# Kernel optimization log

Hardware: AMD Instinct MI355X
Metric: run time of the kernel (lower is better)

The kernel has to match this reference:

```python
import jax, jax.numpy as jnp
import numpy as np

NUM_GRAPHS = 1024
NODES_PER_GRAPH = 116
DEG = 32
IN_CH = 116
HID = 32
EPS = 1e-5


def setup_inputs() -> dict:
    key = jax.random.key(0)
    ks = jax.random.split(key, 16)
    N = NUM_GRAPHS * NODES_PER_GRAPH
    E = N * DEG
    x = jax.random.normal(ks[0], (N, IN_CH), dtype=jnp.float32)
    # edges stay within each graph: graph id per edge, then random src/dst node in that graph
    gid = jnp.arange(E, dtype=jnp.int64) // (NODES_PER_GRAPH * DEG)
    off = gid * NODES_PER_GRAPH
    src = off + jax.random.randint(ks[1], (E,), 0, NODES_PER_GRAPH, dtype=jnp.int64)
    dst = off + jax.random.randint(ks[2], (E,), 0, NODES_PER_GRAPH, dtype=jnp.int64)
    edge_index = jnp.stack([src, dst], axis=0)
    edge_weight = jax.random.uniform(ks[3], (E,), dtype=jnp.float32)
    batch = jnp.arange(N, dtype=jnp.int64) // NODES_PER_GRAPH
    xavier = lambda k, fi, fo: jax.random.uniform(k, (fi, fo), jnp.float32, -1.0, 1.0) * np.sqrt(6.0 / (fi + fo))
    return {
        "x": x, "edge_index": edge_index, "edge_weight": edge_weight, "batch": batch,
        "W1": xavier(ks[4], IN_CH, HID), "b1": jnp.zeros((HID,), jnp.float32),
        "g1": jnp.ones((HID,), jnp.float32), "be1": jnp.zeros((HID,), jnp.float32),
        "W2": xavier(ks[5], HID, 2 * HID), "b2": jnp.zeros((2 * HID,), jnp.float32),
        "g2": jnp.ones((2 * HID,), jnp.float32), "be2": jnp.zeros((2 * HID,), jnp.float32),
        "Wf1": xavier(ks[6], 4 * HID, HID), "bf1": jnp.zeros((HID,), jnp.float32),
        "gf": jnp.ones((HID,), jnp.float32), "bef": jnp.zeros((HID,), jnp.float32),
        "Wf2": xavier(ks[7], HID, 2), "bf2": jnp.zeros((2,), jnp.float32),
    }


def _gcn_conv(x, row, col, ew, W, b):
    """PyG GCNConv: linear -> add self-loops -> sym-normalized scatter-add -> +bias."""
    N = x.shape[0]
    h = x @ W  # [N, out]
    loop = jnp.arange(N, dtype=row.dtype)
    row_sl = jnp.concatenate([row, loop])
    col_sl = jnp.concatenate([col, loop])
    w_sl = jnp.concatenate([ew, jnp.ones((N,), ew.dtype)])
    deg = jax.ops.segment_sum(w_sl, col_sl, num_segments=N)
    dinv = jnp.where(deg > 0, jax.lax.rsqrt(deg), 0.0)
    norm = dinv[row_sl] * w_sl * dinv[col_sl]  # [E+N]
    msg = h[row_sl] * norm[:, None]            # gather + scale
    out = jax.ops.segment_sum(msg, col_sl, num_segments=N)
    return out + b


def _bn(x, g, b):
    # BatchNorm1d in training mode: biased batch stats over axis 0
    m = jnp.mean(x, axis=0)
    v = jnp.mean(jnp.square(x - m), axis=0)
    return (x - m) * jax.lax.rsqrt(v + EPS) * g + b


def reference(x, edge_index, edge_weight, batch, W1, b1, g1, be1, W2, b2, g2, be2,
              Wf1, bf1, gf, bef, Wf2, bf2):
    row, col = edge_index[0], edge_index[1]
    h = jax.nn.relu(_bn(_gcn_conv(x, row, col, edge_weight, W1, b1), g1, be1))
    h = jax.nn.relu(_bn(_gcn_conv(h, row, col, edge_weight, W2, b2), g2, be2))
    # global mean / max pool over graphs
    counts = jax.ops.segment_sum(jnp.ones((h.shape[0],), h.dtype), batch, num_segments=NUM_GRAPHS)
    x_mean = jax.ops.segment_sum(h, batch, num_segments=NUM_GRAPHS) / counts[:, None]
    x_max = jax.ops.segment_max(h, batch, num_segments=NUM_GRAPHS)
    emb = jnp.concatenate([x_mean, x_max], axis=1)  # [G, 4*HID]
    z = jax.nn.relu(_bn(emb @ Wf1 + bf1, gf, bef))  # dropout = identity (eval)
    return z @ Wf2 + bf2  # [G, num_classes]
```

## Files before the change

### kernel.cpp

```cpp
#include <hip/hip_runtime.h>

#define NPG 116
#define EPG (NPG * 32)
#define HID 32
#define HID2 64
#define EPS 1e-5f

#define AS 136
#define YSS 40
#define HPG 7424

using bf16x8 = __attribute__((ext_vector_type(8))) short;
using f32x4  = __attribute__((ext_vector_type(4))) float;

__device__ __forceinline__ unsigned short f2bf(float f) {
  union { float f; unsigned int i; } cv;
  cv.f = f;
  unsigned int x = cv.i;
  x += 0x7fff + ((x >> 16) & 1);
  return (unsigned short)(x >> 16);
}

#define MFMA16(a, b, c) __builtin_amdgcn_mfma_f32_16x16x32_bf16((a), (b), (c), 0, 0, 0)


__global__ __launch_bounds__(1024) void k_build(const int* __restrict__ ei,
                                                const float* __restrict__ ew,
                                                float* __restrict__ dinvg,
                                                float* __restrict__ buf,
                                                int N, int E) {
  __shared__ float Wf[NPG * NPG];
  __shared__ float degs[NPG];
  const int g = blockIdx.x, tid = threadIdx.x;
  const int nb = g * NPG, e0 = g * EPG;
  const int* rowp = ei;
  const int* colp = ei + E;

  for (int i = tid; i < NPG; i += 1024) degs[i] = 1.0f;
  { float4* p = (float4*)Wf;
    for (int i = tid; i < NPG * 29; i += 1024) p[i] = make_float4(0,0,0,0); }
  __syncthreads();

  for (int e = tid; e < EPG; e += 1024) {
    int eg = e0 + e;
    int s = rowp[eg] - nb, d = colp[eg] - nb;
    float wv = ew[eg];
    atomicAdd(&degs[d], wv);
    atomicAdd(&Wf[d * NPG + s], wv);
  }
  if (tid < NPG) atomicAdd(&Wf[tid * NPG + tid], 1.0f);
  __syncthreads();

  if (tid < NPG) dinvg[nb + tid] = rsqrtf(degs[tid]);
  int* wbg = (int*)(buf + (size_t)g * HPG);
  for (int idx = tid; idx < NPG * 64; idx += 1024) {
    int r = idx >> 6, jj = idx & 63;
    int val = 0;
    if (jj < 58) {
      float2 v = *(const float2*)&Wf[r * NPG + 2 * jj];
      val = (unsigned)f2bf(v.x) | ((unsigned)f2bf(v.y) << 16);
    }
    wbg[idx] = val;
  }
}

__global__ __launch_bounds__(256) void k_conv1(const float* __restrict__ x,
                                               const float* __restrict__ W1,
                                               const float* __restrict__ dinvg,
                                               const float* __restrict__ buf,
                                               float* __restrict__ h1,
                                               float* __restrict__ stats,
                                               int N) {
  __shared__ __align__(16) short W1T[HID * AS];
  __shared__ __align__(16) short L1T[HID * AS];
  __shared__ float dv[NPG];
  __shared__ float ss[HID], qs[HID];
  const int g = blockIdx.x, tid = threadIdx.x;
  const int nb = g * NPG;
  const int l = tid & 63, w = tid >> 6;
  const int rf = l & 15, kg = l >> 4;

  if (tid < HID) { ss[tid] = 0.0f; qs[tid] = 0.0f; }
  for (int i = tid; i < NPG; i += 256) dv[i] = dinvg[nb + i];
  for (int i = tid; i < HID * 20; i += 256) {
    int c = i / 20, k = 116 + (i - 20 * (i / 20));
    W1T[c * AS + k] = 0;
    L1T[c * AS + k] = 0;
  }
  for (int i = tid; i < NPG * HID; i += 256) {
    int k = i >> 5, c = i & 31;
    W1T[c * AS + k] = (short)f2bf(W1[i]);
  }
  __syncthreads();

#pragma unroll
  for (int mi = 0; mi < 2; ++mi) {
    const int mt = w + 4 * mi;
    const int rl = mt * 16 + rf;
    f32x4 a0 = {0.f,0.f,0.f,0.f}, a1 = {0.f,0.f,0.f,0.f};
#pragma unroll
    for (int kk = 0; kk < 4; ++kk) {
      bf16x8 a;
      if (rl < NPG) {
        const float* xr = x + (size_t)(nb + rl) * NPG;
        if (kk < 3) {
          const float4* xp = (const float4*)(xr + kk * 32 + kg * 8);
          float4 v0 = xp[0], v1 = xp[1];
          a[0] = (short)f2bf(v0.x); a[1] = (short)f2bf(v0.y);
          a[2] = (short)f2bf(v0.z); a[3] = (short)f2bf(v0.w);
          a[4] = (short)f2bf(v1.x); a[5] = (short)f2bf(v1.y);
          a[6] = (short)f2bf(v1.z); a[7] = (short)f2bf(v1.w);
        } else {
          const int k0 = 96 + kg * 8;
#pragma unroll
          for (int j = 0; j < 8; ++j) {
            int k = k0 + j;
            a[j] = (k < NPG) ? (short)f2bf(xr[k]) : (short)0;
          }
        }
      } else {
#pragma unroll
        for (int j = 0; j < 8; ++j) a[j] = 0;
      }
      bf16x8 b0 = *(const bf16x8*)&W1T[rf * AS + kk * 32 + kg * 8];
      bf16x8 b1 = *(const bf16x8*)&W1T[(16 + rf) * AS + kk * 32 + kg * 8];
      a0 = MFMA16(a, b0, a0);
      a1 = MFMA16(a, b1, a1);
    }
#pragma unroll
    for (int i = 0; i < 4; ++i) {
      int row = mt * 16 + kg * 4 + i;
      if (row < NPG) {
        float dr = dv[row];
        L1T[rf * AS + row] = (short)f2bf(dr * a0[i]);
        L1T[(16 + rf) * AS + row] = (short)f2bf(dr * a1[i]);
      }
    }
  }
  __syncthreads();

  const unsigned short* wbs =
      (const unsigned short*)(buf + (size_t)g * HPG);
  float s0 = 0.f, q0 = 0.f, s1 = 0.f, q1 = 0.f;
#pragma unroll
  for (int mi = 0; mi < 2; ++mi) {
    const int mt = w + 4 * mi;
    const int rl = mt * 16 + rf;
    f32x4 a0 = {0.f,0.f,0.f,0.f}, a1 = {0.f,0.f,0.f,0.f};
#pragma unroll
    for (int kk = 0; kk < 4; ++kk) {
      bf16x8 a;
      if (rl < NPG) {
        a = *(const bf16x8*)&wbs[rl * 128 + kk * 32 + kg * 8];
      } else {
#pragma unroll
        for (int j = 0; j < 8; ++j) a[j] = 0;
      }
      bf16x8 b0 = *(const bf16x8*)&L1T[rf * AS + kk * 32 + kg * 8];
      bf16x8 b1 = *(const bf16x8*)&L1T[(16 + rf) * AS + kk * 32 + kg * 8];
      a0 = MFMA16(a, b0, a0);
      a1 = MFMA16(a, b1, a1);
    }
#pragma unroll
    for (int i = 0; i < 4; ++i) {
      int row = mt * 16 + kg * 4 + i;
      if (row < NPG) {
        float dr = dv[row];
        float v0 = dr * a0[i], v1 = dr * a1[i];
        float* hrow = h1 + (size_t)(nb + row) * HID;
        hrow[rf] = v0;
        hrow[16 + rf] = v1;
        s0 += v0; q0 += v0 * v0;
        s1 += v1; q1 += v1 * v1;
      }
    }
  }
  atomicAdd(&ss[rf], s0);      atomicAdd(&qs[rf], q0);
  atomicAdd(&ss[16 + rf], s1); atomicAdd(&qs[16 + rf], q1);
  __syncthreads();
  if (tid < HID) {
    atomicAdd(&stats[tid], ss[tid]);
    atomicAdd(&stats[32 + tid], qs[tid]);
  }
}

__global__ __launch_bounds__(512) void k_conv2(const float* __restrict__ h1,
                                               const float* __restrict__ W2,
                                               const float* __restrict__ g1,
                                               const float* __restrict__ be1,
                                               const float* __restrict__ stats,
                                               const float* __restrict__ dinvg,
                                               float* __restrict__ buf,
                                               float* __restrict__ stats2,
                                               float invN, int N) {
  __shared__ __align__(16) short ysb[128 * YSS];
  __shared__ __align__(16) short W2T[HID2 * YSS];
  __shared__ __align__(16) short L2T[HID2 * AS];
  __shared__ float dv[NPG];
  __shared__ float ss[HID2], qs[HID2];
  __shared__ float a1s[HID], c1s[HID];
  const int g = blockIdx.x, tid = threadIdx.x;
  const int nb = g * NPG;
  const int l = tid & 63, w = tid >> 6;
  const int rf = l & 15, kg = l >> 4;
  float* bufg = buf + (size_t)g * HPG;

  if (tid < HID) {
    float m = stats[tid] * invN;
    float v = stats[32 + tid] * invN - m * m;
    float a = g1[tid] * rsqrtf(v + EPS);
    a1s[tid] = a;
    c1s[tid] = be1[tid] - m * a;
  }
  if (tid < HID2) { ss[tid] = 0.0f; qs[tid] = 0.0f; }
  { int* p = (int*)ysb;
    for (int i = tid; i < 128 * YSS / 2; i += 512) p[i] = 0; }
  { int* p = (int*)L2T;
    for (int i = tid; i < HID2 * AS / 2; i += 512) p[i] = 0; }
  for (int i = tid; i < HID * HID2; i += 512) {
    int k = i >> 6, c = i & 63;
    W2T[c * YSS + k] = (short)f2bf(W2[i]);
  }
  for (int i = tid; i < NPG; i += 512) dv[i] = dinvg[nb + i];
  __syncthreads();

  {
    const float4* hg = (const float4*)(h1 + (size_t)nb * HID);
    for (int i = tid; i < NPG * 8; i += 512) {
      int r = i >> 3, kc = i & 7, k0 = kc * 4;
      float4 hv = hg[i];
      float dr = dv[r];
      float y0 = dr * fmaxf(0.f, a1s[k0 + 0] * hv.x + c1s[k0 + 0]);
      float y1 = dr * fmaxf(0.f, a1s[k0 + 1] * hv.y + c1s[k0 + 1]);
      float y2 = dr * fmaxf(0.f, a1s[k0 + 2] * hv.z + c1s[k0 + 2]);
      float y3 = dr * fmaxf(0.f, a1s[k0 + 3] * hv.w + c1s[k0 + 3]);
      unsigned int* yp = (unsigned int*)&ysb[r * YSS + k0];
      yp[0] = (unsigned)f2bf(y0) | ((unsigned)f2bf(y1) << 16);
      yp[1] = (unsigned)f2bf(y2) | ((unsigned)f2bf(y3) << 16);
    }
  }
  __syncthreads();

#pragma unroll
  for (int u = 0; u < 4; ++u) {
    const int t = w + 8 * u;
    const int mt = t >> 2, nt = t & 3;
    bf16x8 a = *(const bf16x8*)&ysb[(mt * 16 + rf) * YSS + kg * 8];
    bf16x8 b = *(const bf16x8*)&W2T[(nt * 16 + rf) * YSS + kg * 8];
    f32x4 acc = {0.f, 0.f, 0.f, 0.f};
    acc = MFMA16(a, b, acc);
    const int col = nt * 16 + rf;
#pragma unroll
    for (int i = 0; i < 4; ++i) {
      int row = mt * 16 + kg * 4 + i;
      if (row < NPG) L2T[col * AS + row] = (short)f2bf(acc[i]);
    }
  }
  __syncthreads();

  {
    const unsigned short* wbs = (const unsigned short*)bufg;
    const int mt = w;
    const int rl = mt * 16 + rf;
    f32x4 acc[4];
#pragma unroll
    for (int nt = 0; nt < 4; ++nt) acc[nt] = (f32x4){0.f, 0.f, 0.f, 0.f};
#pragma unroll
    for (int kk = 0; kk < 4; ++kk) {
      bf16x8 a;
      if (rl < NPG) {
        a = *(const bf16x8*)&wbs[rl * 128 + kk * 32 + kg * 8];
      } else {
#pragma unroll
        for (int j = 0; j < 8; ++j) a[j] = 0;
      }
#pragma unroll
      for (int nt = 0; nt < 4; ++nt) {
        bf16x8 b = *(const bf16x8*)&L2T[(nt * 16 + rf) * AS + kk * 32 + kg * 8];
        acc[nt] = MFMA16(a, b, acc[nt]);
      }
    }
#pragma unroll
    for (int nt = 0; nt < 4; ++nt) {
      const int col = nt * 16 + rf;
      float s_ = 0.f, q_ = 0.f;
#pragma unroll
      for (int i = 0; i < 4; ++i) {
        int row = mt * 16 + kg * 4 + i;
        if (row < NPG) {
          float v = dv[row] * acc[nt][i];
          bufg[row * HID2 + col] = v;
          s_ += v; q_ += v * v;
        }
      }
      atomicAdd(&ss[col], s_);
      atomicAdd(&qs[col], q_);
    }
  }
  __syncthreads();
  if (tid < HID2) {
    atomicAdd(&stats2[tid], ss[tid]);
    atomicAdd(&stats2[64 + tid], qs[tid]);
  }
}

__global__ __launch_bounds__(256) void k_pool(const float* __restrict__ buf,
                                              const float* __restrict__ g2,
                                              const float* __restrict__ be2,
                                              const float* __restrict__ stats2,
                                              const float* __restrict__ Wf1,
                                              float* __restrict__ z,
                                              float invN, int N) {
  __shared__ float4 psum4[256], pmax4[256];
  __shared__ __align__(16) float emb[128];
  __shared__ __align__(16) float a2s[HID2], c2s[HID2];
  int g = blockIdx.x, tid = threadIdx.x;
  if (tid < HID2) {
    float m = stats2[tid] * invN;
    float v = stats2[64 + tid] * invN - m * m;
    float a = g2[tid] * rsqrtf(v + EPS);
    a2s[tid] = a;
    c2s[tid] = be2[tid] - m * a;
  }
  __syncthreads();
  int c4 = tid & 15, rg = tid >> 4;
  float4 av = ((const float4*)a2s)[c4], bv = ((const float4*)c2s)[c4];
  const float4* h4 = (const float4*)(buf + (size_t)g * HPG);
  float4 s = {0.f, 0.f, 0.f, 0.f};
  float4 mx = {-1e30f, -1e30f, -1e30f, -1e30f};
  for (int n = rg; n < NPG; n += 16) {
    float4 v = h4[n * 16 + c4];
    float4 y;
    y.x = fmaxf(0.f, av.x * v.x + bv.x);
    y.y = fmaxf(0.f, av.y * v.y + bv.y);
    y.z = fmaxf(0.f, av.z * v.z + bv.z);
    y.w = fmaxf(0.f, av.w * v.w + bv.w);
    s.x += y.x; s.y += y.y; s.z += y.z; s.w += y.w;
    mx.x = fmaxf(mx.x, y.x); mx.y = fmaxf(mx.y, y.y);
    mx.z = fmaxf(mx.z, y.z); mx.w = fmaxf(mx.w, y.w);
  }
  psum4[rg * 16 + c4] = s;
  pmax4[rg * 16 + c4] = mx;
  __syncthreads();
  if (tid < 16) {
    float4 S = psum4[tid], M = pmax4[tid];
    for (int j = 1; j < 16; ++j) {
      float4 p = psum4[j * 16 + tid], q = pmax4[j * 16 + tid];
      S.x += p.x; S.y += p.y; S.z += p.z; S.w += p.w;
      M.x = fmaxf(M.x, q.x); M.y = fmaxf(M.y, q.y);
      M.z = fmaxf(M.z, q.z); M.w = fmaxf(M.w, q.w);
    }
    const float inv = 1.0f / NPG;
    ((float4*)emb)[tid] = make_float4(S.x * inv, S.y * inv, S.z * inv, S.w * inv);
    ((float4*)emb)[16 + tid] = M;
  }
  __syncthreads();
  if (tid < 32) {
    float acc = 0.0f;
#pragma unroll
    for (int k = 0; k < 128; ++k) acc += emb[k] * Wf1[k * 32 + tid];
    z[g * 32 + tid] = acc;
  }
}

__global__ __launch_bounds__(256) void k_final(const float* __restrict__ z,
                                               const float* __restrict__ gf,
                                               const float* __restrict__ bef,
                                               const float* __restrict__ Wf2,
                                               const float* __restrict__ bf2,
                                               float* __restrict__ out, int G) {
  __shared__ float ss[32], qs[32], af[32], cf[32];
  __shared__ float w2s[64], b2s[2];
  int tid = threadIdx.x;
  if (tid < 32) { ss[tid] = 0.0f; qs[tid] = 0.0f; }
  if (tid < 64) w2s[tid] = Wf2[tid];
  if (tid < 2) b2s[tid] = bf2[tid];
  __syncthreads();
  const float4* z4 = (const float4*)z;
  int n4 = G * 8;
  float4 s = {0.f, 0.f, 0.f, 0.f}, q = {0.f, 0.f, 0.f, 0.f};
  for (int i = tid; i < n4; i += 256) {
    float4 v = z4[i];
    s.x += v.x; s.y += v.y; s.z += v.z; s.w += v.w;
    q.x += v.x * v.x; q.y += v.y * v.y; q.z += v.z * v.z; q.w += v.w * v.w;
  }
  int cg = (tid & 7) * 4;
  atomicAdd(&ss[cg + 0], s.x); atomicAdd(&ss[cg + 1], s.y);
  atomicAdd(&ss[cg + 2], s.z); atomicAdd(&ss[cg + 3], s.w);
  atomicAdd(&qs[cg + 0], q.x); atomicAdd(&qs[cg + 1], q.y);
  atomicAdd(&qs[cg + 2], q.z); atomicAdd(&qs[cg + 3], q.w);
  __syncthreads();
  if (tid < 32) {
    float invG = 1.0f / G;
    float m = ss[tid] * invG;
    float v = qs[tid] * invG - m * m;
    float a = gf[tid] * rsqrtf(v + EPS);
    af[tid] = a;
    cf[tid] = bef[tid] - m * a;
  }
  __syncthreads();
  for (int g = tid; g < G; g += 256) {
    float o0 = b2s[0], o1 = b2s[1];
    const float4* zr = z4 + g * 8;
#pragma unroll
    for (int kc = 0; kc < 8; ++kc) {
      float4 v = zr[kc];
      int j = 4 * kc;
      float y;
      y = fmaxf(0.f, af[j + 0] * v.x + cf[j + 0]);
      o0 += y * w2s[2 * (j + 0)]; o1 += y * w2s[2 * (j + 0) + 1];
      y = fmaxf(0.f, af[j + 1] * v.y + cf[j + 1]);
      o0 += y * w2s[2 * (j + 1)]; o1 += y * w2s[2 * (j + 1) + 1];
      y = fmaxf(0.f, af[j + 2] * v.z + cf[j + 2]);
      o0 += y * w2s[2 * (j + 2)]; o1 += y * w2s[2 * (j + 2) + 1];
      y = fmaxf(0.f, af[j + 3] * v.w + cf[j + 3]);
      o0 += y * w2s[2 * (j + 3)]; o1 += y * w2s[2 * (j + 3) + 1];
    }
    out[g * 2] = o0;
    out[g * 2 + 1] = o1;
  }
}

extern "C" void kernel_launch(void* const* d_in, const int* in_sizes, int n_in,
                              void* d_out, int out_size, void* d_ws, size_t ws_size,
                              hipStream_t stream) {
  const float* x   = (const float*)d_in[0];
  const int*   ei  = (const int*)d_in[1];
  const float* ew  = (const float*)d_in[2];
  const float* W1  = (const float*)d_in[4];
  const float* g1  = (const float*)d_in[6];
  const float* be1 = (const float*)d_in[7];
  const float* W2  = (const float*)d_in[8];
  const float* g2  = (const float*)d_in[10];
  const float* be2 = (const float*)d_in[11];
  const float* Wf1 = (const float*)d_in[12];
  const float* gf  = (const float*)d_in[14];
  const float* bef = (const float*)d_in[15];
  const float* Wf2 = (const float*)d_in[16];
  const float* bf2 = (const float*)d_in[17];

  int N = in_sizes[3];
  int E = in_sizes[2];
  int G = N / NPG;

  float* ws    = (float*)d_ws;
  float* stats = ws;
  float* dinv  = ws + 256;
  float* h1    = dinv + N;
  float* buf   = h1 + (size_t)N * HID;
  float* z     = buf + (size_t)G * HPG;
  float* out   = (float*)d_out;
  float invN   = 1.0f / (float)N;

  hipMemsetAsync(stats, 0, 256 * sizeof(float), stream);
  k_build<<<G, 1024, 0, stream>>>(ei, ew, dinv, buf, N, E);
  k_conv1<<<G, 256, 0, stream>>>(x, W1, dinv, buf, h1, stats, N);
  k_conv2<<<G, 512, 0, stream>>>(h1, W2, g1, be1, stats, dinv, buf,
                                 stats + 64, invN, N);
  k_pool<<<G, 256, 0, stream>>>(buf, g2, be2, stats + 64, Wf1, z, invN, N);
  k_final<<<1, 256, 0, stream>>>(z, gf, bef, Wf2, bf2, out, G);
}
```

Baseline: 173.7 us.

## Prefetch global loads before LDS setup and widen conv1 to one tile per wave

In k_build, edge indices and weights are loaded into registers before shared memory is zeroed, and the bf16 adjacency is written with 16-byte stores instead of 4-byte stores. k_conv1 now launches 512 threads so each wave owns one 16-row tile, and it issues its x-row loads and adjacency-fragment loads before the shared-memory setup and barrier. k_conv2 likewise prefetches its adjacency A fragments into registers at kernel start. The aim is to hide global-memory latency behind LDS initialisation and to add parallelism, at the cost of more registers per thread.

```diff
diff --git a/kernel.cpp b/kernel.cpp
--- a/kernel.cpp
+++ b/kernel.cpp
@@ -36,35 +36,51 @@
   const int* rowp = ei;
   const int* colp = ei + E;
 
+  int sarr[4], darr[4];
+  float warr[4];
+#pragma unroll
+  for (int u = 0; u < 4; ++u) {
+    int e = tid + u * 1024;
+    bool ok = e < EPG;
+    sarr[u] = ok ? rowp[e0 + e] - nb : 0;
+    darr[u] = ok ? colp[e0 + e] - nb : 0;
+    warr[u] = ok ? ew[e0 + e] : 0.0f;
+  }
   for (int i = tid; i < NPG; i += 1024) degs[i] = 1.0f;
   { float4* p = (float4*)Wf;
     for (int i = tid; i < NPG * 29; i += 1024) p[i] = make_float4(0,0,0,0); }
   __syncthreads();
 
-  for (int e = tid; e < EPG; e += 1024) {
-    int eg = e0 + e;
-    int s = rowp[eg] - nb, d = colp[eg] - nb;
-    float wv = ew[eg];
-    atomicAdd(&degs[d], wv);
-    atomicAdd(&Wf[d * NPG + s], wv);
+#pragma unroll
+  for (int u = 0; u < 4; ++u) {
+    if (tid + u * 1024 < EPG) {
+      atomicAdd(&degs[darr[u]], warr[u]);
+      atomicAdd(&Wf[darr[u] * NPG + sarr[u]], warr[u]);
+    }
   }
   if (tid < NPG) atomicAdd(&Wf[tid * NPG + tid], 1.0f);
   __syncthreads();
 
   if (tid < NPG) dinvg[nb + tid] = rsqrtf(degs[tid]);
-  int* wbg = (int*)(buf + (size_t)g * HPG);
-  for (int idx = tid; idx < NPG * 64; idx += 1024) {
-    int r = idx >> 6, jj = idx & 63;
-    int val = 0;
-    if (jj < 58) {
-      float2 v = *(const float2*)&Wf[r * NPG + 2 * jj];
-      val = (unsigned)f2bf(v.x) | ((unsigned)f2bf(v.y) << 16);
-    }
-    wbg[idx] = val;
-  }
-}
-
-__global__ __launch_bounds__(256) void k_conv1(const float* __restrict__ x,
+  int4* wb4 = (int4*)(buf + (size_t)g * HPG);
+  for (int idx = tid; idx < NPG * 16; idx += 1024) {
+    int r = idx >> 4, j8 = (idx & 15) * 8;
+    float vb[8];
+#pragma unroll
+    for (int t = 0; t < 8; ++t) {
+      int c = j8 + t;
+      vb[t] = (c < NPG) ? Wf[r * NPG + c] : 0.0f;
+    }
+    int4 val;
+    val.x = (unsigned)f2bf(vb[0]) | ((unsigned)f2bf(vb[1]) << 16);
+    val.y = (unsigned)f2bf(vb[2]) | ((unsigned)f2bf(vb[3]) << 16);
+    val.z = (unsigned)f2bf(vb[4]) | ((unsigned)f2bf(vb[5]) << 16);
+    val.w = (unsigned)f2bf(vb[6]) | ((unsigned)f2bf(vb[7]) << 16);
+    wb4[idx] = val;
+  }
+}
+
+__global__ __launch_bounds__(512) void k_conv1(const float* __restrict__ x,
                                                const float* __restrict__ W1,
                                                const float* __restrict__ dinvg,
                                                const float* __restrict__ buf,
@@ -79,44 +95,52 @@
   const int nb = g * NPG;
   const int l = tid & 63, w = tid >> 6;
   const int rf = l & 15, kg = l >> 4;
-
+  const int mt = w, rl = mt * 16 + rf;
+
+  float4 xv[6];
+  float xt[8];
+  {
+    const float* xr = x + (size_t)(nb + (rl < NPG ? rl : 0)) * NPG;
+    const float4* xp4 = (const float4*)xr;
+#pragma unroll
+    for (int kk = 0; kk < 3; ++kk) {
+      xv[2 * kk]     = xp4[kk * 8 + kg * 2];
+      xv[2 * kk + 1] = xp4[kk * 8 + kg * 2 + 1];
+    }
+#pragma unroll
+    for (int j = 0; j < 8; ++j) {
+      int k = 96 + kg * 8 + j;
+      xt[j] = (k < NPG) ? xr[k] : 0.0f;
+    }
+  }
   if (tid < HID) { ss[tid] = 0.0f; qs[tid] = 0.0f; }
-  for (int i = tid; i < NPG; i += 256) dv[i] = dinvg[nb + i];
-  for (int i = tid; i < HID * 20; i += 256) {
+  for (int i = tid; i < NPG; i += 512) dv[i] = dinvg[nb + i];
+  for (int i = tid; i < HID * 20; i += 512) {
     int c = i / 20, k = 116 + (i - 20 * (i / 20));
     W1T[c * AS + k] = 0;
     L1T[c * AS + k] = 0;
   }
-  for (int i = tid; i < NPG * HID; i += 256) {
+  for (int i = tid; i < NPG * HID; i += 512) {
     int k = i >> 5, c = i & 31;
     W1T[c * AS + k] = (short)f2bf(W1[i]);
   }
   __syncthreads();
 
-#pragma unroll
-  for (int mi = 0; mi < 2; ++mi) {
-    const int mt = w + 4 * mi;
-    const int rl = mt * 16 + rf;
+  {
     f32x4 a0 = {0.f,0.f,0.f,0.f}, a1 = {0.f,0.f,0.f,0.f};
 #pragma unroll
     for (int kk = 0; kk < 4; ++kk) {
       bf16x8 a;
       if (rl < NPG) {
-        const float* xr = x + (size_t)(nb + rl) * NPG;
         if (kk < 3) {
-          const float4* xp = (const float4*)(xr + kk * 32 + kg * 8);
-          float4 v0 = xp[0], v1 = xp[1];
+          float4 v0 = xv[2 * kk], v1 = xv[2 * kk + 1];
           a[0] = (short)f2bf(v0.x); a[1] = (short)f2bf(v0.y);
           a[2] = (short)f2bf(v0.z); a[3] = (short)f2bf(v0.w);
           a[4] = (short)f2bf(v1.x); a[5] = (short)f2bf(v1.y);
           a[6] = (short)f2bf(v1.z); a[7] = (short)f2bf(v1.w);
         } else {
-          const int k0 = 96 + kg * 8;
-#pragma unroll
-          for (int j = 0; j < 8; ++j) {
-            int k = k0 + j;
-            a[j] = (k < NPG) ? (short)f2bf(xr[k]) : (short)0;
-          }
+#pragma unroll
+          for (int j = 0; j < 8; ++j) a[j] = (short)f2bf(xt[j]);
         }
       } else {
 #pragma unroll
@@ -137,30 +161,33 @@
       }
     }
   }
-  __syncthreads();
-
-  const unsigned short* wbs =
-      (const unsigned short*)(buf + (size_t)g * HPG);
-  float s0 = 0.f, q0 = 0.f, s1 = 0.f, q1 = 0.f;
-#pragma unroll
-  for (int mi = 0; mi < 2; ++mi) {
-    const int mt = w + 4 * mi;
-    const int rl = mt * 16 + rf;
+  bf16x8 av[4];
+  {
+    const unsigned short* wbs =
+        (const unsigned short*)(buf + (size_t)g * HPG);
+    const int rs = (rl < NPG ? rl : 0) * 128;
+#pragma unroll
+    for (int kk = 0; kk < 4; ++kk)
+      av[kk] = *(const bf16x8*)&wbs[rs + kk * 32 + kg * 8];
+    if (rl >= NPG) {
+#pragma unroll
+      for (int kk = 0; kk < 4; ++kk)
+#pragma unroll
+        for (int j = 0; j < 8; ++j) av[kk][j] = 0;
+    }
+  }
+  __syncthreads();
+
+  {
     f32x4 a0 = {0.f,0.f,0.f,0.f}, a1 = {0.f,0.f,0.f,0.f};
 #pragma unroll
     for (int kk = 0; kk < 4; ++kk) {
-      bf16x8 a;
-      if (rl < NPG) {
-        a = *(const bf16x8*)&wbs[rl * 128 + kk * 32 + kg * 8];
-      } else {
-#pragma unroll
-        for (int j = 0; j < 8; ++j) a[j] = 0;
-      }
       bf16x8 b0 = *(const bf16x8*)&L1T[rf * AS + kk * 32 + kg * 8];
       bf16x8 b1 = *(const bf16x8*)&L1T[(16 + rf) * AS + kk * 32 + kg * 8];
-      a0 = MFMA16(a, b0, a0);
-      a1 = MFMA16(a, b1, a1);
-    }
+      a0 = MFMA16(av[kk], b0, a0);
+      a1 = MFMA16(av[kk], b1, a1);
+    }
+    float s0 = 0.f, q0 = 0.f, s1 = 0.f, q1 = 0.f;
 #pragma unroll
     for (int i = 0; i < 4; ++i) {
       int row = mt * 16 + kg * 4 + i;
@@ -174,9 +201,9 @@
         s1 += v1; q1 += v1 * v1;
       }
     }
-  }
-  atomicAdd(&ss[rf], s0);      atomicAdd(&qs[rf], q0);
-  atomicAdd(&ss[16 + rf], s1); atomicAdd(&qs[16 + rf], q1);
+    atomicAdd(&ss[rf], s0);      atomicAdd(&qs[rf], q0);
+    atomicAdd(&ss[16 + rf], s1); atomicAdd(&qs[16 + rf], q1);
+  }
   __syncthreads();
   if (tid < HID) {
     atomicAdd(&stats[tid], ss[tid]);
@@ -204,7 +231,22 @@
   const int l = tid & 63, w = tid >> 6;
   const int rf = l & 15, kg = l >> 4;
   float* bufg = buf + (size_t)g * HPG;
-
+  const int mt = w, rl = mt * 16 + rf;
+
+  bf16x8 av[4];
+  {
+    const unsigned short* wbs = (const unsigned short*)bufg;
+    const int rs = (rl < NPG ? rl : 0) * 128;
+#pragma unroll
+    for (int kk = 0; kk < 4; ++kk)
+      av[kk] = *(const bf16x8*)&wbs[rs + kk * 32 + kg * 8];
+    if (rl >= NPG) {
+#pragma unroll
+      for (int kk = 0; kk < 4; ++kk)
+#pragma unroll
+        for (int j = 0; j < 8; ++j) av[kk][j] = 0;
+    }
+  }
   if (tid < HID) {
     float m = stats[tid] * invN;
     float v = stats[32 + tid] * invN - m * m;
@@ -244,40 +286,30 @@
 #pragma unroll
   for (int u = 0; u < 4; ++u) {
     const int t = w + 8 * u;
-    const int mt = t >> 2, nt = t & 3;
-    bf16x8 a = *(const bf16x8*)&ysb[(mt * 16 + rf) * YSS + kg * 8];
+    const int mt2 = t >> 2, nt = t & 3;
+    bf16x8 a = *(const bf16x8*)&ysb[(mt2 * 16 + rf) * YSS + kg * 8];
     bf16x8 b = *(const bf16x8*)&W2T[(nt * 16 + rf) * YSS + kg * 8];
     f32x4 acc = {0.f, 0.f, 0.f, 0.f};
     acc = MFMA16(a, b, acc);
     const int col = nt * 16 + rf;
 #pragma unroll
     for (int i = 0; i < 4; ++i) {
-      int row = mt * 16 + kg * 4 + i;
+      int row = mt2 * 16 + kg * 4 + i;
       if (row < NPG) L2T[col * AS + row] = (short)f2bf(acc[i]);
     }
   }
   __syncthreads();
 
   {
-    const unsigned short* wbs = (const unsigned short*)bufg;
-    const int mt = w;
-    const int rl = mt * 16 + rf;
     f32x4 acc[4];
 #pragma unroll
     for (int nt = 0; nt < 4; ++nt) acc[nt] = (f32x4){0.f, 0.f, 0.f, 0.f};
 #pragma unroll
     for (int kk = 0; kk < 4; ++kk) {
-      bf16x8 a;
-      if (rl < NPG) {
-        a = *(const bf16x8*)&wbs[rl * 128 + kk * 32 + kg * 8];
-      } else {
-#pragma unroll
-        for (int j = 0; j < 8; ++j) a[j] = 0;
-      }
 #pragma unroll
       for (int nt = 0; nt < 4; ++nt) {
         bf16x8 b = *(const bf16x8*)&L2T[(nt * 16 + rf) * AS + kk * 32 + kg * 8];
-        acc[nt] = MFMA16(a, b, acc[nt]);
+        acc[nt] = MFMA16(av[kk], b, acc[nt]);
       }
     }
 #pragma unroll
@@ -454,7 +486,7 @@
 
   hipMemsetAsync(stats, 0, 256 * sizeof(float), stream);
   k_build<<<G, 1024, 0, stream>>>(ei, ew, dinv, buf, N, E);
-  k_conv1<<<G, 256, 0, stream>>>(x, W1, dinv, buf, h1, stats, N);
+  k_conv1<<<G, 512, 0, stream>>>(x, W1, dinv, buf, h1, stats, N);
   k_conv2<<<G, 512, 0, stream>>>(h1, W2, g1, be1, stats, dinv, buf,
                                  stats + 64, invN, N);
   k_pool<<<G, 256, 0, stream>>>(buf, g2, be2, stats + 64, Wf1, z, invN, N);
```

After: 162.6 us. -6.4%, faster.

## Fuse all GNN stages into one cooperative kernel with register-resident activations

Applied to the files above, without the earlier changes.

Replaces the five-kernel pipeline with one cooperative kernel. Each 512-thread block handles four graphs and keeps the bf16 adjacency fragments and conv outputs in registers across stages, so the h1, h2, adjacency and z buffers no longer round-trip through global memory. Grid-wide syncs stand in for the kernel boundaries around the three batch-norm statistic reductions. In exchange it carries heavy register pressure, only 256 blocks in flight, and the cost of three grid barriers.

```diff
diff --git a/kernel.cpp b/kernel.cpp
--- a/kernel.cpp
+++ b/kernel.cpp
@@ -1,14 +1,15 @@
 #include <hip/hip_runtime.h>
+#include <hip/hip_cooperative_groups.h>
+namespace cg = cooperative_groups;
 
 #define NPG 116
 #define EPG (NPG * 32)
 #define HID 32
 #define HID2 64
 #define EPS 1e-5f
-
 #define AS 136
 #define YSS 40
-#define HPG 7424
+#define NG 4
 
 using bf16x8 = __attribute__((ext_vector_type(8))) short;
 using f32x4  = __attribute__((ext_vector_type(4))) float;
@@ -23,401 +24,333 @@
 
 #define MFMA16(a, b, c) __builtin_amdgcn_mfma_f32_16x16x32_bf16((a), (b), (c), 0, 0, 0)
 
-
-__global__ __launch_bounds__(1024) void k_build(const int* __restrict__ ei,
-                                                const float* __restrict__ ew,
-                                                float* __restrict__ dinvg,
-                                                float* __restrict__ buf,
-                                                int N, int E) {
-  __shared__ float Wf[NPG * NPG];
-  __shared__ float degs[NPG];
-  const int g = blockIdx.x, tid = threadIdx.x;
-  const int nb = g * NPG, e0 = g * EPG;
-  const int* rowp = ei;
-  const int* colp = ei + E;
-
-  for (int i = tid; i < NPG; i += 1024) degs[i] = 1.0f;
-  { float4* p = (float4*)Wf;
-    for (int i = tid; i < NPG * 29; i += 1024) p[i] = make_float4(0,0,0,0); }
-  __syncthreads();
-
-  for (int e = tid; e < EPG; e += 1024) {
-    int eg = e0 + e;
-    int s = rowp[eg] - nb, d = colp[eg] - nb;
-    float wv = ew[eg];
-    atomicAdd(&degs[d], wv);
-    atomicAdd(&Wf[d * NPG + s], wv);
-  }
-  if (tid < NPG) atomicAdd(&Wf[tid * NPG + tid], 1.0f);
-  __syncthreads();
-
-  if (tid < NPG) dinvg[nb + tid] = rsqrtf(degs[tid]);
-  int* wbg = (int*)(buf + (size_t)g * HPG);
-  for (int idx = tid; idx < NPG * 64; idx += 1024) {
-    int r = idx >> 6, jj = idx & 63;
-    int val = 0;
-    if (jj < 58) {
-      float2 v = *(const float2*)&Wf[r * NPG + 2 * jj];
-      val = (unsigned)f2bf(v.x) | ((unsigned)f2bf(v.y) << 16);
-    }
-    wbg[idx] = val;
-  }
-}
-
-__global__ __launch_bounds__(256) void k_conv1(const float* __restrict__ x,
-                                               const float* __restrict__ W1,
-                                               const float* __restrict__ dinvg,
-                                               const float* __restrict__ buf,
-                                               float* __restrict__ h1,
-                                               float* __restrict__ stats,
-                                               int N) {
+__global__ __launch_bounds__(512, 2) void k_fused(
+    const float* __restrict__ x, const int* __restrict__ ei,
+    const float* __restrict__ ew, const float* __restrict__ W1,
+    const float* __restrict__ W2, const float* __restrict__ Wf1,
+    const float* __restrict__ Wf2, const float* __restrict__ g1,
+    const float* __restrict__ be1, const float* __restrict__ g2,
+    const float* __restrict__ be2, const float* __restrict__ gf,
+    const float* __restrict__ bef, const float* __restrict__ bf2,
+    float* __restrict__ stats, float* __restrict__ out, int N, int E) {
+  __shared__ __align__(16) char regA[NPG * NPG * 4];
   __shared__ __align__(16) short W1T[HID * AS];
   __shared__ __align__(16) short L1T[HID * AS];
-  __shared__ float dv[NPG];
-  __shared__ float ss[HID], qs[HID];
-  const int g = blockIdx.x, tid = threadIdx.x;
-  const int nb = g * NPG;
+  __shared__ float dv[NG][NPG];
+  __shared__ float ssq[128];
+  __shared__ float cfs[256];
+  __shared__ float emb[NG][128];
+  __shared__ float zloc[NG * 32];
+  __shared__ float psum[64];
+  __shared__ int   pmaxi[64];
+
+  float* Wf  = (float*)regA;
+  short* ysb = (short*)regA;
+  short* W2T = (short*)(regA + 10240);
+  short* L2T = (short*)(regA + 15360);
+
+  cg::grid_group grid = cg::this_grid();
+  const int tid = threadIdx.x;
   const int l = tid & 63, w = tid >> 6;
   const int rf = l & 15, kg = l >> 4;
-
-  if (tid < HID) { ss[tid] = 0.0f; qs[tid] = 0.0f; }
-  for (int i = tid; i < NPG; i += 256) dv[i] = dinvg[nb + i];
-  for (int i = tid; i < HID * 20; i += 256) {
-    int c = i / 20, k = 116 + (i - 20 * (i / 20));
-    W1T[c * AS + k] = 0;
-    L1T[c * AS + k] = 0;
-  }
-  for (int i = tid; i < NPG * HID; i += 256) {
-    int k = i >> 5, c = i & 31;
-    W1T[c * AS + k] = (short)f2bf(W1[i]);
-  }
-  __syncthreads();
-
-#pragma unroll
-  for (int mi = 0; mi < 2; ++mi) {
-    const int mt = w + 4 * mi;
-    const int rl = mt * 16 + rf;
-    f32x4 a0 = {0.f,0.f,0.f,0.f}, a1 = {0.f,0.f,0.f,0.f};
+  const int rl = w * 16 + rf;
+  const bool rok = rl < NPG;
+  const int g0 = NG * blockIdx.x;
+  const float invN = 1.0f / (float)N;
+
+  for (int i = tid; i < HID * AS / 2; i += 512) {
+    ((int*)W1T)[i] = 0;
+    ((int*)L1T)[i] = 0;
+  }
+  __syncthreads();
+  for (int i = tid; i < NPG * 8; i += 512) {
+    int k = i >> 3, c4 = (i & 7) * 4;
+    float4 v = ((const float4*)W1)[i];
+    W1T[(c4 + 0) * AS + k] = (short)f2bf(v.x);
+    W1T[(c4 + 1) * AS + k] = (short)f2bf(v.y);
+    W1T[(c4 + 2) * AS + k] = (short)f2bf(v.z);
+    W1T[(c4 + 3) * AS + k] = (short)f2bf(v.w);
+  }
+
+  bf16x8 av[NG][4];
+  f32x4 h1a[NG][2];
+
+#pragma unroll
+  for (int gi = 0; gi < NG; ++gi) {
+    const int g = g0 + gi, nb = g * NPG, e0 = g * EPG;
+    float* degs = emb[gi];
+    for (int i = tid; i < NPG; i += 512) degs[i] = 1.0f;
+    { float4* p = (float4*)Wf;
+      for (int i = tid; i < NPG * 29; i += 512) p[i] = make_float4(0,0,0,0); }
+    __syncthreads();
+    for (int vi = tid; vi < EPG / 4; vi += 512) {
+      int4 s4 = ((const int4*)(ei + e0))[vi];
+      int4 d4 = ((const int4*)(ei + E + e0))[vi];
+      float4 w4 = ((const float4*)(ew + e0))[vi];
+      atomicAdd(&degs[d4.x - nb], w4.x);
+      atomicAdd(&Wf[(d4.x - nb) * NPG + (s4.x - nb)], w4.x);
+      atomicAdd(&degs[d4.y - nb], w4.y);
+      atomicAdd(&Wf[(d4.y - nb) * NPG + (s4.y - nb)], w4.y);
+      atomicAdd(&degs[d4.z - nb], w4.z);
+      atomicAdd(&Wf[(d4.z - nb) * NPG + (s4.z - nb)], w4.z);
+      atomicAdd(&degs[d4.w - nb], w4.w);
+      atomicAdd(&Wf[(d4.w - nb) * NPG + (s4.w - nb)], w4.w);
+    }
+    if (tid < NPG) atomicAdd(&Wf[tid * (NPG + 1)], 1.0f);
+    __syncthreads();
+    if (tid < NPG) dv[gi][tid] = rsqrtf(degs[tid]);
+
 #pragma unroll
     for (int kk = 0; kk < 4; ++kk) {
+      int off = kk * 32 + kg * 8;
       bf16x8 a;
-      if (rl < NPG) {
-        const float* xr = x + (size_t)(nb + rl) * NPG;
-        if (kk < 3) {
-          const float4* xp = (const float4*)(xr + kk * 32 + kg * 8);
-          float4 v0 = xp[0], v1 = xp[1];
+#pragma unroll
+      for (int j = 0; j < 8; ++j) {
+        int c = off + j;
+        float v = (rok && c < NPG) ? Wf[rl * NPG + c] : 0.0f;
+        a[j] = (short)f2bf(v);
+      }
+      av[gi][kk] = a;
+    }
+    f32x4 a0 = {0.f,0.f,0.f,0.f}, a1v = {0.f,0.f,0.f,0.f};
+    {
+      const float* xr = x + (size_t)(nb + (rok ? rl : 0)) * NPG;
+#pragma unroll
+      for (int kk = 0; kk < 4; ++kk) {
+        int off = kk * 32 + kg * 8;
+        bf16x8 a;
+        if (rok && off + 8 <= NPG) {
+          float4 v0 = *(const float4*)(xr + off);
+          float4 v1 = *(const float4*)(xr + off + 4);
           a[0] = (short)f2bf(v0.x); a[1] = (short)f2bf(v0.y);
           a[2] = (short)f2bf(v0.z); a[3] = (short)f2bf(v0.w);
           a[4] = (short)f2bf(v1.x); a[5] = (short)f2bf(v1.y);
           a[6] = (short)f2bf(v1.z); a[7] = (short)f2bf(v1.w);
         } else {
-          const int k0 = 96 + kg * 8;
 #pragma unroll
           for (int j = 0; j < 8; ++j) {
-            int k = k0 + j;
-            a[j] = (k < NPG) ? (short)f2bf(xr[k]) : (short)0;
+            int c = off + j;
+            a[j] = (rok && c < NPG) ? (short)f2bf(xr[c]) : (short)0;
           }
         }
-      } else {
-#pragma unroll
-        for (int j = 0; j < 8; ++j) a[j] = 0;
-      }
-      bf16x8 b0 = *(const bf16x8*)&W1T[rf * AS + kk * 32 + kg * 8];
-      bf16x8 b1 = *(const bf16x8*)&W1T[(16 + rf) * AS + kk * 32 + kg * 8];
-      a0 = MFMA16(a, b0, a0);
-      a1 = MFMA16(a, b1, a1);
-    }
+        bf16x8 b0 = *(const bf16x8*)&W1T[rf * AS + off];
+        bf16x8 b1 = *(const bf16x8*)&W1T[(16 + rf) * AS + off];
+        a0 = MFMA16(a, b0, a0);
+        a1v = MFMA16(a, b1, a1v);
+      }
+    }
+    __syncthreads();
 #pragma unroll
     for (int i = 0; i < 4; ++i) {
-      int row = mt * 16 + kg * 4 + i;
+      int row = w * 16 + kg * 4 + i;
       if (row < NPG) {
-        float dr = dv[row];
+        float dr = dv[gi][row];
         L1T[rf * AS + row] = (short)f2bf(dr * a0[i]);
-        L1T[(16 + rf) * AS + row] = (short)f2bf(dr * a1[i]);
-      }
-    }
-  }
-  __syncthreads();
-
-  const unsigned short* wbs =
-      (const unsigned short*)(buf + (size_t)g * HPG);
-  float s0 = 0.f, q0 = 0.f, s1 = 0.f, q1 = 0.f;
-#pragma unroll
-  for (int mi = 0; mi < 2; ++mi) {
-    const int mt = w + 4 * mi;
-    const int rl = mt * 16 + rf;
-    f32x4 a0 = {0.f,0.f,0.f,0.f}, a1 = {0.f,0.f,0.f,0.f};
+        L1T[(16 + rf) * AS + row] = (short)f2bf(dr * a1v[i]);
+      }
+    }
+    __syncthreads();
+    f32x4 h0 = {0.f,0.f,0.f,0.f}, h1v = {0.f,0.f,0.f,0.f};
 #pragma unroll
     for (int kk = 0; kk < 4; ++kk) {
-      bf16x8 a;
-      if (rl < NPG) {
-        a = *(const bf16x8*)&wbs[rl * 128 + kk * 32 + kg * 8];
-      } else {
-#pragma unroll
-        for (int j = 0; j < 8; ++j) a[j] = 0;
-      }
       bf16x8 b0 = *(const bf16x8*)&L1T[rf * AS + kk * 32 + kg * 8];
       bf16x8 b1 = *(const bf16x8*)&L1T[(16 + rf) * AS + kk * 32 + kg * 8];
-      a0 = MFMA16(a, b0, a0);
-      a1 = MFMA16(a, b1, a1);
-    }
-#pragma unroll
-    for (int i = 0; i < 4; ++i) {
-      int row = mt * 16 + kg * 4 + i;
-      if (row < NPG) {
-        float dr = dv[row];
-        float v0 = dr * a0[i], v1 = dr * a1[i];
-        float* hrow = h1 + (size_t)(nb + row) * HID;
-        hrow[rf] = v0;
-        hrow[16 + rf] = v1;
-        s0 += v0; q0 += v0 * v0;
-        s1 += v1; q1 += v1 * v1;
-      }
-    }
-  }
-  atomicAdd(&ss[rf], s0);      atomicAdd(&qs[rf], q0);
-  atomicAdd(&ss[16 + rf], s1); atomicAdd(&qs[16 + rf], q1);
+      h0 = MFMA16(av[gi][kk], b0, h0);
+      h1v = MFMA16(av[gi][kk], b1, h1v);
+    }
+    h1a[gi][0] = h0;
+    h1a[gi][1] = h1v;
+    __syncthreads();
+  }
+
+  for (int i = tid; i < 2560; i += 512) ((int*)regA)[i] = 0;
+  for (int i = tid; i < 4352; i += 512) ((int*)(regA + 15360))[i] = 0;
+  if (tid < 512) {
+    int k = tid >> 4, c4 = (tid & 15) * 4;
+    float4 v = ((const float4*)W2)[tid];
+    W2T[(c4 + 0) * YSS + k] = (short)f2bf(v.x);
+    W2T[(c4 + 1) * YSS + k] = (short)f2bf(v.y);
+    W2T[(c4 + 2) * YSS + k] = (short)f2bf(v.z);
+    W2T[(c4 + 3) * YSS + k] = (short)f2bf(v.w);
+  }
+  if (tid < 64) { ssq[tid] = 0.f; ssq[64 + tid] = 0.f; }
+  __syncthreads();
+  {
+    float s0 = 0.f, q0 = 0.f, s1 = 0.f, q1 = 0.f;
+#pragma unroll
+    for (int gi = 0; gi < NG; ++gi)
+#pragma unroll
+      for (int i = 0; i < 4; ++i) {
+        int row = w * 16 + kg * 4 + i;
+        if (row < NPG) {
+          float dr = dv[gi][row];
+          float v0 = dr * h1a[gi][0][i], v1 = dr * h1a[gi][1][i];
+          s0 += v0; q0 += v0 * v0;
+          s1 += v1; q1 += v1 * v1;
+        }
+      }
+    atomicAdd(&ssq[rf], s0);      atomicAdd(&ssq[64 + rf], q0);
+    atomicAdd(&ssq[16 + rf], s1); atomicAdd(&ssq[80 + rf], q1);
+  }
   __syncthreads();
   if (tid < HID) {
-    atomicAdd(&stats[tid], ss[tid]);
-    atomicAdd(&stats[32 + tid], qs[tid]);
-  }
-}
-
-__global__ __launch_bounds__(512) void k_conv2(const float* __restrict__ h1,
-                                               const float* __restrict__ W2,
-                                               const float* __restrict__ g1,
-                                               const float* __restrict__ be1,
-                                               const float* __restrict__ stats,
-                                               const float* __restrict__ dinvg,
-                                               float* __restrict__ buf,
-                                               float* __restrict__ stats2,
-                                               float invN, int N) {
-  __shared__ __align__(16) short ysb[128 * YSS];
-  __shared__ __align__(16) short W2T[HID2 * YSS];
-  __shared__ __align__(16) short L2T[HID2 * AS];
-  __shared__ float dv[NPG];
-  __shared__ float ss[HID2], qs[HID2];
-  __shared__ float a1s[HID], c1s[HID];
-  const int g = blockIdx.x, tid = threadIdx.x;
-  const int nb = g * NPG;
-  const int l = tid & 63, w = tid >> 6;
-  const int rf = l & 15, kg = l >> 4;
-  float* bufg = buf + (size_t)g * HPG;
+    atomicAdd(&stats[tid], ssq[tid]);
+    atomicAdd(&stats[32 + tid], ssq[64 + tid]);
+  }
+  grid.sync();
 
   if (tid < HID) {
     float m = stats[tid] * invN;
     float v = stats[32 + tid] * invN - m * m;
     float a = g1[tid] * rsqrtf(v + EPS);
-    a1s[tid] = a;
-    c1s[tid] = be1[tid] - m * a;
-  }
-  if (tid < HID2) { ss[tid] = 0.0f; qs[tid] = 0.0f; }
-  { int* p = (int*)ysb;
-    for (int i = tid; i < 128 * YSS / 2; i += 512) p[i] = 0; }
-  { int* p = (int*)L2T;
-    for (int i = tid; i < HID2 * AS / 2; i += 512) p[i] = 0; }
-  for (int i = tid; i < HID * HID2; i += 512) {
-    int k = i >> 6, c = i & 63;
-    W2T[c * YSS + k] = (short)f2bf(W2[i]);
-  }
-  for (int i = tid; i < NPG; i += 512) dv[i] = dinvg[nb + i];
-  __syncthreads();
-
-  {
-    const float4* hg = (const float4*)(h1 + (size_t)nb * HID);
-    for (int i = tid; i < NPG * 8; i += 512) {
-      int r = i >> 3, kc = i & 7, k0 = kc * 4;
-      float4 hv = hg[i];
-      float dr = dv[r];
-      float y0 = dr * fmaxf(0.f, a1s[k0 + 0] * hv.x + c1s[k0 + 0]);
-      float y1 = dr * fmaxf(0.f, a1s[k0 + 1] * hv.y + c1s[k0 + 1]);
-      float y2 = dr * fmaxf(0.f, a1s[k0 + 2] * hv.z + c1s[k0 + 2]);
-      float y3 = dr * fmaxf(0.f, a1s[k0 + 3] * hv.w + c1s[k0 + 3]);
-      unsigned int* yp = (unsigned int*)&ysb[r * YSS + k0];
-      yp[0] = (unsigned)f2bf(y0) | ((unsigned)f2bf(y1) << 16);
-      yp[1] = (unsigned)f2bf(y2) | ((unsigned)f2bf(y3) << 16);
-    }
-  }
-  __syncthreads();
-
-#pragma unroll
-  for (int u = 0; u < 4; ++u) {
-    const int t = w + 8 * u;
-    const int mt = t >> 2, nt = t & 3;
-    bf16x8 a = *(const bf16x8*)&ysb[(mt * 16 + rf) * YSS + kg * 8];
-    bf16x8 b = *(const bf16x8*)&W2T[(nt * 16 + rf) * YSS + kg * 8];
-    f32x4 acc = {0.f, 0.f, 0.f, 0.f};
-    acc = MFMA16(a, b, acc);
-    const int col = nt * 16 + rf;
+    cfs[tid] = a;
+    cfs[32 + tid] = be1[tid] - m * a;
+  }
+  if (tid < 64) { ssq[tid] = 0.f; ssq[64 + tid] = 0.f; }
+  __syncthreads();
+
+  f32x4 h2a[NG][4];
+#pragma unroll
+  for (int gi = 0; gi < NG; ++gi) {
 #pragma unroll
     for (int i = 0; i < 4; ++i) {
-      int row = mt * 16 + kg * 4 + i;
-      if (row < NPG) L2T[col * AS + row] = (short)f2bf(acc[i]);
-    }
-  }
-  __syncthreads();
-
-  {
-    const unsigned short* wbs = (const unsigned short*)bufg;
-    const int mt = w;
-    const int rl = mt * 16 + rf;
-    f32x4 acc[4];
-#pragma unroll
-    for (int nt = 0; nt < 4; ++nt) acc[nt] = (f32x4){0.f, 0.f, 0.f, 0.f};
+      int row = w * 16 + kg * 4 + i;
+      if (row < NPG) {
+        float dr = dv[gi][row];
+        float hv0 = dr * h1a[gi][0][i], hv1 = dr * h1a[gi][1][i];
+        float y0 = dr * fmaxf(0.f, cfs[rf] * hv0 + cfs[32 + rf]);
+        float y1 = dr * fmaxf(0.f, cfs[16 + rf] * hv1 + cfs[48 + rf]);
+        ysb[row * YSS + rf] = (short)f2bf(y0);
+        ysb[row * YSS + 16 + rf] = (short)f2bf(y1);
+      }
+    }
+    __syncthreads();
+#pragma unroll
+    for (int u = 0; u < 4; ++u) {
+      int t = w + 8 * u;
+      int mt2 = t >> 2, nt = t & 3;
+      bf16x8 a = *(const bf16x8*)&ysb[(mt2 * 16 + rf) * YSS + kg * 8];
+      bf16x8 bb = *(const bf16x8*)&W2T[(nt * 16 + rf) * YSS + kg * 8];
+      f32x4 acc = {0.f, 0.f, 0.f, 0.f};
+      acc = MFMA16(a, bb, acc);
+      int col = nt * 16 + rf;
+#pragma unroll
+      for (int i = 0; i < 4; ++i) {
+        int row = mt2 * 16 + kg * 4 + i;
+        if (row < NPG) L2T[col * AS + row] = (short)f2bf(acc[i]);
+      }
+    }
+    __syncthreads();
+#pragma unroll
+    for (int nt = 0; nt < 4; ++nt) h2a[gi][nt] = (f32x4){0.f,0.f,0.f,0.f};
 #pragma unroll
     for (int kk = 0; kk < 4; ++kk) {
-      bf16x8 a;
-      if (rl < NPG) {
-        a = *(const bf16x8*)&wbs[rl * 128 + kk * 32 + kg * 8];
-      } else {
-#pragma unroll
-        for (int j = 0; j < 8; ++j) a[j] = 0;
-      }
 #pragma unroll
       for (int nt = 0; nt < 4; ++nt) {
-        bf16x8 b = *(const bf16x8*)&L2T[(nt * 16 + rf) * AS + kk * 32 + kg * 8];
-        acc[nt] = MFMA16(a, b, acc[nt]);
-      }
-    }
-#pragma unroll
-    for (int nt = 0; nt < 4; ++nt) {
-      const int col = nt * 16 + rf;
-      float s_ = 0.f, q_ = 0.f;
+        bf16x8 bb = *(const bf16x8*)&L2T[(nt * 16 + rf) * AS + kk * 32 + kg * 8];
+        h2a[gi][nt] = MFMA16(av[gi][kk], bb, h2a[gi][nt]);
+      }
+    }
+    __syncthreads();
+  }
+#pragma unroll
+  for (int nt = 0; nt < 4; ++nt) {
+    float s_ = 0.f, q_ = 0.f;
+#pragma unroll
+    for (int gi = 0; gi < NG; ++gi)
 #pragma unroll
       for (int i = 0; i < 4; ++i) {
-        int row = mt * 16 + kg * 4 + i;
+        int row = w * 16 + kg * 4 + i;
         if (row < NPG) {
-          float v = dv[row] * acc[nt][i];
-          bufg[row * HID2 + col] = v;
+          float v = dv[gi][row] * h2a[gi][nt][i];
           s_ += v; q_ += v * v;
         }
       }
-      atomicAdd(&ss[col], s_);
-      atomicAdd(&qs[col], q_);
-    }
+    atomicAdd(&ssq[nt * 16 + rf], s_);
+    atomicAdd(&ssq[64 + nt * 16 + rf], q_);
   }
   __syncthreads();
   if (tid < HID2) {
-    atomicAdd(&stats2[tid], ss[tid]);
-    atomicAdd(&stats2[64 + tid], qs[tid]);
-  }
-}
-
-__global__ __launch_bounds__(256) void k_pool(const float* __restrict__ buf,
-                                              const float* __restrict__ g2,
-                                              const float* __restrict__ be2,
-                                              const float* __restrict__ stats2,
-                                              const float* __restrict__ Wf1,
-                                              float* __restrict__ z,
-                                              float invN, int N) {
-  __shared__ float4 psum4[256], pmax4[256];
-  __shared__ __align__(16) float emb[128];
-  __shared__ __align__(16) float a2s[HID2], c2s[HID2];
-  int g = blockIdx.x, tid = threadIdx.x;
+    atomicAdd(&stats[64 + tid], ssq[tid]);
+    atomicAdd(&stats[128 + tid], ssq[64 + tid]);
+  }
+  grid.sync();
+
   if (tid < HID2) {
-    float m = stats2[tid] * invN;
-    float v = stats2[64 + tid] * invN - m * m;
+    float m = stats[64 + tid] * invN;
+    float v = stats[128 + tid] * invN - m * m;
     float a = g2[tid] * rsqrtf(v + EPS);
-    a2s[tid] = a;
-    c2s[tid] = be2[tid] - m * a;
-  }
-  __syncthreads();
-  int c4 = tid & 15, rg = tid >> 4;
-  float4 av = ((const float4*)a2s)[c4], bv = ((const float4*)c2s)[c4];
-  const float4* h4 = (const float4*)(buf + (size_t)g * HPG);
-  float4 s = {0.f, 0.f, 0.f, 0.f};
-  float4 mx = {-1e30f, -1e30f, -1e30f, -1e30f};
-  for (int n = rg; n < NPG; n += 16) {
-    float4 v = h4[n * 16 + c4];
-    float4 y;
-    y.x = fmaxf(0.f, av.x * v.x + bv.x);
-    y.y = fmaxf(0.f, av.y * v.y + bv.y);
-    y.z = fmaxf(0.f, av.z * v.z + bv.z);
-    y.w = fmaxf(0.f, av.w * v.w + bv.w);
-    s.x += y.x; s.y += y.y; s.z += y.z; s.w += y.w;
-    mx.x = fmaxf(mx.x, y.x); mx.y = fmaxf(mx.y, y.y);
-    mx.z = fmaxf(mx.z, y.z); mx.w = fmaxf(mx.w, y.w);
-  }
-  psum4[rg * 16 + c4] = s;
-  pmax4[rg * 16 + c4] = mx;
-  __syncthreads();
-  if (tid < 16) {
-    float4 S = psum4[tid], M = pmax4[tid];
-    for (int j = 1; j < 16; ++j) {
-      float4 p = psum4[j * 16 + tid], q = pmax4[j * 16 + tid];
-      S.x += p.x; S.y += p.y; S.z += p.z; S.w += p.w;
-      M.x = fmaxf(M.x, q.x); M.y = fmaxf(M.y, q.y);
-      M.z = fmaxf(M.z, q.z); M.w = fmaxf(M.w, q.w);
-    }
-    const float inv = 1.0f / NPG;
-    ((float4*)emb)[tid] = make_float4(S.x * inv, S.y * inv, S.z * inv, S.w * inv);
-    ((float4*)emb)[16 + tid] = M;
+    cfs[64 + tid] = a;
+    cfs[128 + tid] = be2[tid] - m * a;
+  }
+  __syncthreads();
+#pragma unroll
+  for (int gi = 0; gi < NG; ++gi) {
+    if (tid < 64) { psum[tid] = 0.f; pmaxi[tid] = 0; }
+    __syncthreads();
+#pragma unroll
+    for (int nt = 0; nt < 4; ++nt) {
+      int col = nt * 16 + rf;
+      float a2 = cfs[64 + col], c2 = cfs[128 + col];
+      float s_ = 0.f, mx = 0.f;
+#pragma unroll
+      for (int i = 0; i < 4; ++i) {
+        int row = w * 16 + kg * 4 + i;
+        if (row < NPG) {
+          float hv = dv[gi][row] * h2a[gi][nt][i];
+          float y = fmaxf(0.f, a2 * hv + c2);
+          s_ += y; mx = fmaxf(mx, y);
+        }
+      }
+      atomicAdd(&psum[col], s_);
+      atomicMax(&pmaxi[col], __float_as_int(mx));
+    }
+    __syncthreads();
+    if (tid < 64) {
+      emb[gi][tid] = psum[tid] * (1.0f / NPG);
+      emb[gi][64 + tid] = __int_as_float(pmaxi[tid]);
+    }
+    __syncthreads();
+  }
+  if (tid < NG * 32) {
+    int gi = tid >> 5, c = tid & 31;
+    float acc = 0.f;
+#pragma unroll
+    for (int k = 0; k < 128; ++k) acc += emb[gi][k] * Wf1[k * 32 + c];
+    zloc[tid] = acc;
   }
   __syncthreads();
   if (tid < 32) {
-    float acc = 0.0f;
-#pragma unroll
-    for (int k = 0; k < 128; ++k) acc += emb[k] * Wf1[k * 32 + tid];
-    z[g * 32 + tid] = acc;
-  }
-}
-
-__global__ __launch_bounds__(256) void k_final(const float* __restrict__ z,
-                                               const float* __restrict__ gf,
-                                               const float* __restrict__ bef,
-                                               const float* __restrict__ Wf2,
-                                               const float* __restrict__ bf2,
-                                               float* __restrict__ out, int G) {
-  __shared__ float ss[32], qs[32], af[32], cf[32];
-  __shared__ float w2s[64], b2s[2];
-  int tid = threadIdx.x;
-  if (tid < 32) { ss[tid] = 0.0f; qs[tid] = 0.0f; }
-  if (tid < 64) w2s[tid] = Wf2[tid];
-  if (tid < 2) b2s[tid] = bf2[tid];
-  __syncthreads();
-  const float4* z4 = (const float4*)z;
-  int n4 = G * 8;
-  float4 s = {0.f, 0.f, 0.f, 0.f}, q = {0.f, 0.f, 0.f, 0.f};
-  for (int i = tid; i < n4; i += 256) {
-    float4 v = z4[i];
-    s.x += v.x; s.y += v.y; s.z += v.z; s.w += v.w;
-    q.x += v.x * v.x; q.y += v.y * v.y; q.z += v.z * v.z; q.w += v.w * v.w;
-  }
-  int cg = (tid & 7) * 4;
-  atomicAdd(&ss[cg + 0], s.x); atomicAdd(&ss[cg + 1], s.y);
-  atomicAdd(&ss[cg + 2], s.z); atomicAdd(&ss[cg + 3], s.w);
-  atomicAdd(&qs[cg + 0], q.x); atomicAdd(&qs[cg + 1], q.y);
-  atomicAdd(&qs[cg + 2], q.z); atomicAdd(&qs[cg + 3], q.w);
-  __syncthreads();
+    float s_ = 0.f, q_ = 0.f;
+#pragma unroll
+    for (int gi = 0; gi < NG; ++gi) {
+      float zv = zloc[gi * 32 + tid];
+      s_ += zv; q_ += zv * zv;
+    }
+    atomicAdd(&stats[192 + tid], s_);
+    atomicAdd(&stats[224 + tid], q_);
+  }
+  grid.sync();
+
   if (tid < 32) {
-    float invG = 1.0f / G;
-    float m = ss[tid] * invG;
-    float v = qs[tid] * invG - m * m;
+    float iG = 1.0f / (float)(NG * gridDim.x);
+    float m = stats[192 + tid] * iG;
+    float v = stats[224 + tid] * iG - m * m;
     float a = gf[tid] * rsqrtf(v + EPS);
-    af[tid] = a;
-    cf[tid] = bef[tid] - m * a;
-  }
-  __syncthreads();
-  for (int g = tid; g < G; g += 256) {
-    float o0 = b2s[0], o1 = b2s[1];
-    const float4* zr = z4 + g * 8;
-#pragma unroll
-    for (int kc = 0; kc < 8; ++kc) {
-      float4 v = zr[kc];
-      int j = 4 * kc;
-      float y;
-      y = fmaxf(0.f, af[j + 0] * v.x + cf[j + 0]);
-      o0 += y * w2s[2 * (j + 0)]; o1 += y * w2s[2 * (j + 0) + 1];
-      y = fmaxf(0.f, af[j + 1] * v.y + cf[j + 1]);
-      o0 += y * w2s[2 * (j + 1)]; o1 += y * w2s[2 * (j + 1) + 1];
-      y = fmaxf(0.f, af[j + 2] * v.z + cf[j + 2]);
-      o0 += y * w2s[2 * (j + 2)]; o1 += y * w2s[2 * (j + 2) + 1];
-      y = fmaxf(0.f, af[j + 3] * v.w + cf[j + 3]);
-      o0 += y * w2s[2 * (j + 3)]; o1 += y * w2s[2 * (j + 3) + 1];
-    }
-    out[g * 2] = o0;
-    out[g * 2 + 1] = o1;
+    cfs[192 + tid] = a;
+    cfs[224 + tid] = bef[tid] - m * a;
+  }
+  __syncthreads();
+  if (tid < NG) {
+    float o0 = bf2[0], o1 = bf2[1];
+#pragma unroll
+    for (int j = 0; j < 32; ++j) {
+      float y = fmaxf(0.f, cfs[192 + j] * zloc[tid * 32 + j] + cfs[224 + j]);
+      o0 += y * Wf2[2 * j];
+      o1 += y * Wf2[2 * j + 1];
+    }
+    out[(g0 + tid) * 2] = o0;
+    out[(g0 + tid) * 2 + 1] = o1;
   }
 }
 
@@ -443,20 +376,13 @@
   int E = in_sizes[2];
   int G = N / NPG;
 
-  float* ws    = (float*)d_ws;
-  float* stats = ws;
-  float* dinv  = ws + 256;
-  float* h1    = dinv + N;
-  float* buf   = h1 + (size_t)N * HID;
-  float* z     = buf + (size_t)G * HPG;
+  float* stats = (float*)d_ws;
   float* out   = (float*)d_out;
-  float invN   = 1.0f / (float)N;
 
   hipMemsetAsync(stats, 0, 256 * sizeof(float), stream);
-  k_build<<<G, 1024, 0, stream>>>(ei, ew, dinv, buf, N, E);
-  k_conv1<<<G, 256, 0, stream>>>(x, W1, dinv, buf, h1, stats, N);
-  k_conv2<<<G, 512, 0, stream>>>(h1, W2, g1, be1, stats, dinv, buf,
-                                 stats + 64, invN, N);
-  k_pool<<<G, 256, 0, stream>>>(buf, g2, be2, stats + 64, Wf1, z, invN, N);
-  k_final<<<1, 256, 0, stream>>>(z, gf, bef, Wf2, bf2, out, G);
+
+  void* args[] = {&x, &ei, &ew, &W1, &W2, &Wf1, &Wf2, &g1, &be1, &g2, &be2,
+                  &gf, &bef, &bf2, &stats, &out, &N, &E};
+  hipLaunchCooperativeKernel((void*)k_fused, dim3(G / NG), dim3(512), args, 0,
+                             stream);
 }
```

New measurement: 186.7 us. 7.5% more time.
